# Performance work log

Measured on AMD Instinct MI355X. Metric: run time of the kernel, lower is better.

Reference implementation:

```python
import jax, jax.numpy as jnp
import numpy as np

LOSS_IDX = jnp.array([0, 1])    # loss_indices from __init__
BASIS_IDX = jnp.array([0, 1])   # dtw_mapping_basis (x, y)


def _dtw_path(cost):
    """Classic DTW DP + backtrack on cost [N, M].
    Returns padded alignment path (a, b) of length N+M-1 with validity mask.
    DP is run as an anti-diagonal wavefront scan (L = N+M-1 steps)."""
    N, M = cost.shape
    L = N + M - 1
    inf = jnp.float32(jnp.inf)
    i_idx = jnp.arange(N)

    def diag_step(carry, k):
        prev1, prev2 = carry  # diagonals k-1 and k-2, indexed by row i
        j = k - i_idx
        valid = (j >= 0) & (j < M)
        c = cost[i_idx, jnp.clip(j, 0, M - 1)]
        up = jnp.concatenate([jnp.full((1,), inf), prev1[:-1]])  # D[i-1, j]
        dg = jnp.concatenate([jnp.full((1,), inf), prev2[:-1]])  # D[i-1, j-1]
        lf = prev1                                               # D[i, j-1]
        best = jnp.minimum(jnp.minimum(up, dg), lf)
        best = jnp.where(jnp.isinf(best), jnp.float32(0.0), best)  # (0,0) seed
        cur = jnp.where(valid, c + best, inf)
        return (cur, prev1), cur

    init = (jnp.full((N,), inf), jnp.full((N,), inf))
    _, diags = jax.lax.scan(diag_step, init, jnp.arange(L))  # [L, N]: D[i,j] = diags[i+j, i]

    def getD(i, j):
        ok = (i >= 0) & (j >= 0)
        return jnp.where(ok, diags[jnp.clip(i + j, 0, L - 1), jnp.clip(i, 0, N - 1)], inf)

    def bt_step(carry, _):
        i, j, done = carry
        emit_valid = jnp.logical_not(done)
        cand = jnp.stack([getD(i - 1, j - 1), getD(i - 1, j), getD(i, j - 1)])
        m = jnp.argmin(cand)  # 0: diag, 1: up, 2: left
        ni = jnp.where(m == 2, i, i - 1)
        nj = jnp.where(m == 1, j, j - 1)
        done2 = done | ((i == 0) & (j == 0))
        ni = jnp.where(done2, 0, ni)
        nj = jnp.where(done2, 0, nj)
        return (ni, nj, done2), (i, j, emit_valid)

    init_bt = (jnp.int32(N - 1), jnp.int32(M - 1), jnp.bool_(False))
    _, (a, b, valid) = jax.lax.scan(bt_step, init_bt, None, length=L)
    return a, b, valid


def _dtw_loss_single(pred, targ, subcoef):
    # DTW alignment is computed on detached (numpy in torch) basis coords.
    p = jax.lax.stop_gradient(pred)[:, BASIS_IDX]
    t = jax.lax.stop_gradient(targ)[:, BASIS_IDX]
    # euclidean pairwise distance cost [N, M]
    cost = jnp.sqrt(jnp.sum((p[:, None, :] - t[None, :, :]) ** 2, axis=-1))
    a, b, valid = _dtw_path(cost)
    d = jnp.abs(pred[a][:, LOSS_IDX] - targ[b][:, LOSS_IDX]) * subcoef  # [L, 2]
    return jnp.sum(d * valid[:, None].astype(d.dtype))


def setup_inputs() -> dict:
    key = jax.random.key(0)
    k1, k2 = jax.random.split(key)
    B, N, M, F = 32, 1024, 1024, 4
    preds = jax.random.normal(k1, (B, N, F), dtype=jnp.float32)
    targs = jax.random.normal(k2, (B, M, F), dtype=jnp.float32)
    subcoef = jnp.ones((2,), dtype=jnp.float32)
    return {"preds": preds, "targs": targs, "subcoef": subcoef}


def reference(preds, targs, subcoef):
    per_sample = jax.vmap(_dtw_loss_single, in_axes=(0, 0, None))(preds, targs, subcoef)
    return jnp.sum(per_sample)
```

## Files before the change

### kernel.cpp

```cpp
#include <hip/hip_runtime.h>
#include <math.h>

#define BATCH 32
#define NN 1024
#define MM 1024
#define LPATH (NN + MM - 1)

#define PB 128
#define PQ 128
#define GB 8
#define GH 8
#define PAN_WORDS 1536
#define BAT_WORDS (GB * GH * PAN_WORDS)
#define DEC_WORDS ((size_t)BATCH * BAT_WORDS)
#define BR_OFFW DEC_WORDS
#define BRPL (9 * 1024)
#define FL_OFFW (BR_OFFW + (size_t)BATCH * BRPL)
#define WS_WORDS (FL_OFFW + (size_t)BATCH * 64)
#define REQ_WS_NEW (WS_WORDS * 4)

#define DEC_WORDS_PER_BATCH ((NN / 4) * (MM / 4))
#define REQ_WS ((size_t)BATCH * DEC_WORDS_PER_BATCH * 4)

__global__ void init_kernel(float* out) { out[0] = 0.0f; }

__global__ void init3(unsigned* __restrict__ wsu, float* __restrict__ out)
{
    const int t = threadIdx.x;
    if (t == 0) out[0] = 0.0f;
    for (int i = t; i < BATCH * 64; i += 256) wsu[FL_OFFW + i] = 0u;
}

__device__ __forceinline__ float wave_shr1(float v)
{
    return __int_as_float(__builtin_amdgcn_update_dpp(
        __float_as_int(v), __float_as_int(v), 0x138, 0xF, 0xF, false));
}

__global__ __launch_bounds__(64, 1) void dtw_dp(
    const float* __restrict__ preds, const float* __restrict__ targs,
    unsigned* __restrict__ wsu)
{
    const int blk = blockIdx.x;
    const int b = blk >> 3, r = blk & 7;
    const int l = threadIdx.x;
    const float INF = __builtin_inff();

    __shared__ __align__(16) float txA[1160], tyA[1160];
    __shared__ __align__(16) float TL[208];
    __shared__ __align__(16) float botL[128];

    for (int i = l; i < 64; i += 64) { txA[i] = 0.f; tyA[i] = 0.f; }
    for (int i = 1087 + l; i < 1160; i += 64) { txA[i] = 0.f; tyA[i] = 0.f; }
    if (l < 16) TL[192 + l] = INF;
    TL[128 + l] = INF;
    if (r == 0) { TL[l] = INF; TL[64 + l] = INF; }

    {
        const float4* tg4 = (const float4*)targs + (size_t)b * MM;
        #pragma unroll
        for (int k = 0; k < 4; ++k) {
            const float4 v = tg4[k * 64 + l];
            const int j = 63 + 4 * (k * 64 + l);
            txA[j] = v.x; tyA[j] = v.y;
            const float4 w = tg4[k * 64 + l];
            (void)w;
        }
    }
    {
        const float4* tg4 = (const float4*)targs + (size_t)b * MM;
        for (int j = l; j < MM; j += 64) {
            const float4 v = tg4[j];
            txA[63 + j] = v.x; tyA[63 + j] = v.y;
        }
    }

    const float4* pp4 = (const float4*)preds + (size_t)b * NN + r * PB;
    const float4 p0 = pp4[2 * l], p1 = pp4[2 * l + 1];
    const float px0 = p0.x, py0 = p0.y, px1 = p1.x, py1 = p1.y;

    unsigned* __restrict__ browI = wsu + BR_OFFW + (size_t)b * BRPL;
    unsigned* __restrict__ flagB = wsu + FL_OFFW + (size_t)b * 64;

    float D0 = INF, D1 = INF;
    __syncthreads();

    for (int c = 0; c < GH; ++c) {
        float tlm1;
        if (r > 0) {
            const int fi = (r - 1) * 8 + c;
            while (__hip_atomic_load(&flagB[fi], __ATOMIC_ACQUIRE,
                                     __HIP_MEMORY_SCOPE_AGENT) == 0u)
                __builtin_amdgcn_s_sleep(1);
            const unsigned* bp = browI + (size_t)r * 1024 + c * PQ;
            TL[2 * l] = __int_as_float(__hip_atomic_load(
                (unsigned*)&bp[2 * l], __ATOMIC_RELAXED, __HIP_MEMORY_SCOPE_AGENT));
            TL[2 * l + 1] = __int_as_float(__hip_atomic_load(
                (unsigned*)&bp[2 * l + 1], __ATOMIC_RELAXED, __HIP_MEMORY_SCOPE_AGENT));
            tlm1 = (c == 0) ? INF
                 : __int_as_float(__hip_atomic_load((unsigned*)&bp[-1],
                       __ATOMIC_RELAXED, __HIP_MEMORY_SCOPE_AGENT));
        } else {
            tlm1 = (c == 0) ? 0.0f : INF;
        }
        const float sh1 = wave_shr1(D1);
        const float dg0init = (l == 0) ? tlm1 : ((c == 0) ? INF : sh1);

        unsigned* __restrict__ decP = wsu + (size_t)b * BAT_WORDS
                                    + (size_t)(r * GH + c) * PAN_WORDS + l;
        const int cb = 63 + c * PQ;

        float txb[8], tyb[8];
        #pragma unroll
        for (int k = 0; k < 4; ++k) {
            txb[k] = txA[cb + k - l]; tyb[k] = tyA[cb + k - l];
        }
        float up0prev = INF;

        for (int it = 0; it < 24; ++it) {
            const int s0 = it * 8;
            const float4 T4a = *(const float4*)&TL[s0];
            const float4 T4b = *(const float4*)&TL[s0 + 4];
            const float Tv[8] = {T4a.x, T4a.y, T4a.z, T4a.w,
                                 T4b.x, T4b.y, T4b.z, T4b.w};
            unsigned word = 0;
            #pragma unroll
            for (int k = 0; k < 8; ++k) {
                const int s = s0 + k;
                const int jq = s - l;
                txb[(k + 4) & 7] = txA[cb + jq + 4];
                tyb[(k + 4) & 7] = tyA[cb + jq + 4];
                const float sh = wave_shr1(D1);
                const float up0 = (l == 0) ? Tv[k] : sh;
                const float dg0 = (jq == 0) ? dg0init : up0prev;
                const float tx = txb[k], ty = tyb[k];
                const float dx0 = px0 - tx, dy0 = py0 - ty;
                const float c0 = __builtin_amdgcn_sqrtf(dx0 * dx0 + dy0 * dy0);
                const float mn0 = fminf(dg0, fminf(up0, D0));
                const float D0n = c0 + mn0;
                const unsigned m0 = (mn0 == dg0) ? 0u : ((mn0 == up0) ? 1u : 2u);
                const float dg1 = D0;
                const float dx1 = px1 - tx, dy1 = py1 - ty;
                const float c1 = __builtin_amdgcn_sqrtf(dx1 * dx1 + dy1 * dy1);
                const float mn1 = fminf(dg1, fminf(D0n, D1));
                const float D1n = c1 + mn1;
                const unsigned m1 = (mn1 == dg1) ? 0u : ((mn1 == D0n) ? 1u : 2u);
                word |= (m0 | (m1 << 2)) << (4 * k);
                const bool act = (jq >= 0) && (jq < PQ);
                if (act) { D0 = D0n; D1 = D1n; }
                up0prev = up0;
                if (l == 63 && act) botL[jq] = D1n;
            }
            decP[it * 64] = word;
        }

        if (r < GB - 1) {
            unsigned* bw = browI + (size_t)(r + 1) * 1024 + c * PQ;
            __hip_atomic_store(&bw[2 * l], __float_as_int(botL[2 * l]),
                               __ATOMIC_RELAXED, __HIP_MEMORY_SCOPE_AGENT);
            __hip_atomic_store(&bw[2 * l + 1], __float_as_int(botL[2 * l + 1]),
                               __ATOMIC_RELAXED, __HIP_MEMORY_SCOPE_AGENT);
            __threadfence();
            if (l == 0)
                __hip_atomic_store(&flagB[r * 8 + c], 1u, __ATOMIC_RELEASE,
                                   __HIP_MEMORY_SCOPE_AGENT);
        }
    }
}

__global__ __launch_bounds__(256, 1) void dtw_bt(
    const float* __restrict__ preds, const float* __restrict__ targs,
    const float* __restrict__ subcoef, const float* __restrict__ ws,
    float* __restrict__ out)
{
    const int b = blockIdx.x, t = threadIdx.x;
    __shared__ float pxA[NN], pyA[NN], txA[MM], tyA[MM];
    __shared__ unsigned path[2048];
    __shared__ int sN;
    __shared__ float wsum[4];

    for (int it = 0; it < 4; ++it) {
        const int idx = it * 256 + t;
        const float4 p4 = ((const float4*)preds)[(size_t)b * NN + idx];
        pxA[idx] = p4.x; pyA[idx] = p4.y;
        const float4 t4 = ((const float4*)targs)[(size_t)b * MM + idx];
        txA[idx] = t4.x; tyA[idx] = t4.y;
    }
    __syncthreads();

    if (t == 0) {
        const unsigned* __restrict__ decB =
            (const unsigned*)ws + (size_t)b * BAT_WORDS;
        int i = NN - 1, j = MM - 1, n = 0;
        int cwidx = -1; unsigned cw = 0;
        while (true) {
            path[n++] = ((unsigned)i << 16) | (unsigned)j;
            if ((i | j) == 0) break;
            const int ll = (i & 127) >> 1;
            const int ss = ll + (j & 127);
            const int widx = (((i >> 7) << 3) + (j >> 7)) * PAN_WORDS
                           + (ss >> 3) * 64 + ll;
            if (widx != cwidx) { cw = decB[widx]; cwidx = widx; }
            const unsigned m = (cw >> ((ss & 7) * 4 + (i & 1) * 2)) & 3u;
            i -= (m != 2u); j -= (m != 1u);
        }
        sN = n;
    }
    __syncthreads();

    const float sc0 = subcoef[0], sc1 = subcoef[1];
    const int n = sN;
    float acc = 0.0f;
    for (int p = t; p < n; p += 256) {
        const unsigned e = path[p];
        const int i = (int)(e >> 16), j = (int)(e & 0xffffu);
        acc += fabsf(pxA[i] - txA[j]) * sc0 + fabsf(pyA[i] - tyA[j]) * sc1;
    }
    #pragma unroll
    for (int o = 32; o > 0; o >>= 1) acc += __shfl_down(acc, o);
    if ((t & 63) == 0) wsum[t >> 6] = acc;
    __syncthreads();
    if (t == 0) atomicAdd(out, (wsum[0] + wsum[1]) + (wsum[2] + wsum[3]));
}

__device__ inline void bt_walk4(const unsigned* __restrict__ sdec, int roff,
                                int iLow, int& i, int& j, int& n,
                                unsigned* __restrict__ path)
{
    int ri = i >> 2, jc = j >> 2;
    unsigned w = sdec[(ri - roff) * 256 + jc];
    while (true) {
        const int base = (ri - roff) * 256 + jc;
        const unsigned wl = sdec[(jc > 0)    ? base - 1   : base];
        const unsigned wu = sdec[(ri > roff) ? base - 256 : base];
        const unsigned wd = sdec[(ri > roff && jc > 0) ? base - 257 : base];
        bool done = false, susp = false;
        while (true) {
            path[n++] = ((unsigned)i << 16) | (unsigned)j;
            if ((i | j) == 0) { done = true; break; }
            const unsigned m = (w >> (((i & 3) * 4 + (j & 3)) * 2)) & 3u;
            i -= (m != 2u); j -= (m != 1u);
            if (i < iLow) { susp = true; break; }
            if ((i >> 2) != ri || (j >> 2) != jc) break;
        }
        if (done || susp) break;
        const int nri = i >> 2, njc = j >> 2;
        w = (nri == ri) ? wl : ((njc == jc) ? wu : wd);
        ri = nri; jc = njc;
    }
}

#define RRL 4
#define CCL 4
#define LANES 64
#define NWAVE 4
#define TPBL (MM / 4)
#define NSUP (TPBL + LANES - 1)
#define LAG 72
#define TOTL (NSUP + (NWAVE - 1) * LAG)
#define DEPTH 32

__global__ __launch_bounds__(256, 1) void dtw_fused_legacy(
    const float* __restrict__ preds, const float* __restrict__ targs,
    const float* __restrict__ subcoef, unsigned* __restrict__ dec,
    float* __restrict__ out)
{
    const int b = blockIdx.x, t = threadIdx.x;
    const int l = t & 63, w = t >> 6;
    const float INF = __builtin_inff();

    __shared__ float pxA[NN], pyA[NN], txA[MM], tyA[MM];
    __shared__ float4 ring[NWAVE - 1][DEPTH];
    __shared__ unsigned sdec[128 * 256];
    __shared__ unsigned path[LPATH + 1];
    __shared__ int sI, sJ, sN;
    __shared__ float wsum[NWAVE];

    for (int it = 0; it < NN / 256; ++it) {
        const int idx = it * 256 + t;
        const float4 p4 = ((const float4*)preds)[(size_t)b * NN + idx];
        pxA[idx] = p4.x; pyA[idx] = p4.y;
        const float4 t4 = ((const float4*)targs)[(size_t)b * MM + idx];
        txA[idx] = t4.x; tyA[idx] = t4.y;
    }
    __syncthreads();

    const int i0 = (w << 8) + (l << 2);
    const float4 px4 = ((const float4*)pxA)[i0 >> 2];
    const float4 py4 = ((const float4*)pyA)[i0 >> 2];
    const float px[RRL] = {px4.x, px4.y, px4.z, px4.w};
    const float py[RRL] = {py4.x, py4.y, py4.z, py4.w};
    unsigned* __restrict__ decW =
        dec + (size_t)b * DEC_WORDS_PER_BATCH + ((size_t)w << 14) + (size_t)l;

    float Dp[RRL], Dbot[CCL], bv[CCL];
    #pragma unroll
    for (int r = 0; r < RRL; ++r) Dp[r] = INF;
    #pragma unroll
    for (int c = 0; c < CCL; ++c) { Dbot[c] = INF; bv[c] = INF; }
    float bndRet = (w == 0 && l == 0) ? 0.0f : INF;
    float4 gcur = make_float4(INF, INF, INF, INF);
    float4 tx4 = ((const float4*)txA)[0], ty4 = ((const float4*)tyA)[0];
    const float4* __restrict__ ringR = ring[(w > 0) ? (w - 1) : 0];

    for (int u = 0; u < TOTL; ++u) {
        const int ul = u - LAG * w;
        if (l == 0) {
            const bool gb = (w > 0) && (ul >= 0) && (ul < TPBL);
            bv[0] = gb ? gcur.x : INF; bv[1] = gb ? gcur.y : INF;
            bv[2] = gb ? gcur.z : INF; bv[3] = gb ? gcur.w : INF;
        }
        const bool act = (ul >= l) && (ul < l + TPBL);
        if (act) {
            const float cx[CCL] = {tx4.x, tx4.y, tx4.z, tx4.w};
            const float cy[CCL] = {ty4.x, ty4.y, ty4.z, ty4.w};
            float cost[RRL][CCL];
            #pragma unroll
            for (int c = 0; c < CCL; ++c)
                #pragma unroll
                for (int r = 0; r < RRL; ++r) {
                    const float dx = px[r] - cx[c], dy = py[r] - cy[c];
                    cost[r][c] = __builtin_amdgcn_sqrtf(dx * dx + dy * dy);
                }
            unsigned word = 0;
            #pragma unroll
            for (int c = 0; c < CCL; ++c) {
                float up = bv[c];
                float dg = (c == 0) ? bndRet : bv[c - 1];
                #pragma unroll
                for (int r = 0; r < RRL; ++r) {
                    const float lf = Dp[r];
                    const unsigned m = (dg <= up && dg <= lf) ? 0u
                                     : ((up <= lf) ? 1u : 2u);
                    const float D = cost[r][c] + fminf(dg, fminf(up, lf));
                    word |= m << ((r * 4 + c) * 2);
                    dg = lf; up = D; Dp[r] = D;
                }
                Dbot[c] = up;
            }
            decW[(ul & 255) << 6] = word;
            if (l == LANES - 1 && w < NWAVE - 1)
                ring[w][ul & (DEPTH - 1)] =
                    make_float4(Dbot[0], Dbot[1], Dbot[2], Dbot[3]);
        }
        bndRet = bv[CCL - 1];
        #pragma unroll
        for (int c = 0; c < CCL; ++c) bv[c] = __shfl_up(Dbot[c], 1);
        const int un = ul + 1;
        if (un >= l && un < l + TPBL) {
            const int jn = CCL * (un - l);
            tx4 = ((const float4*)txA)[jn >> 2];
            ty4 = ((const float4*)tyA)[jn >> 2];
        }
        if (w > 0 && un >= 0 && un < TPBL)
            gcur = ringR[(un + 63) & (DEPTH - 1)];
        if ((u & 7) == 7) __syncthreads();
    }

    __threadfence_block();
    __syncthreads();

    const unsigned* __restrict__ decB = dec + (size_t)b * DEC_WORDS_PER_BATCH;
    {
        const uint4* g4 = (const uint4*)(decB + 32768);
        for (int k = t; k < 8192; k += 256) {
            const uint4 v = g4[k];
            const int kb = k << 2;
            const int wv = kb >> 14;
            const int rem = kb & 16383;
            const int q = rem >> 6;
            const int lb = rem & 63;
            const unsigned wd[4] = {v.x, v.y, v.z, v.w};
            #pragma unroll
            for (int e = 0; e < 4; ++e) {
                const int ll = lb + e;
                const int row = (wv << 6) + ll;
                const int jc = (q - ll) & 255;
                sdec[(row << 8) + jc] = wd[e];
            }
        }
    }
    __syncthreads();
    if (t == 0) {
        int i = NN - 1, j = MM - 1, n = 0;
        bt_walk4(sdec, 128, 512, i, j, n, path);
        sI = i; sJ = j; sN = n;
    }
    __syncthreads();
    {
        const uint4* g4 = (const uint4*)decB;
        for (int k = t; k < 8192; k += 256) {
            const uint4 v = g4[k];
            const int kb = k << 2;
            const int wv = kb >> 14;
            const int rem = kb & 16383;
            const int q = rem >> 6;
            const int lb = rem & 63;
            const unsigned wd[4] = {v.x, v.y, v.z, v.w};
            #pragma unroll
            for (int e = 0; e < 4; ++e) {
                const int ll = lb + e;
                const int row = (wv << 6) + ll;
                const int jc = (q - ll) & 255;
                sdec[(row << 8) + jc] = wd[e];
            }
        }
    }
    __syncthreads();
    if (t == 0) {
        int i = sI, j = sJ, n = sN;
        bt_walk4(sdec, 0, 0, i, j, n, path);
        sN = n;
    }
    __syncthreads();

    const float sc0 = subcoef[0], sc1 = subcoef[1];
    const int n = sN;
    float acc = 0.0f;
    for (int p = t; p < n; p += 256) {
        const unsigned e = path[p];
        const int i = (int)(e >> 16), j = (int)(e & 0xffffu);
        acc += fabsf(pxA[i] - txA[j]) * sc0 + fabsf(pyA[i] - tyA[j]) * sc1;
    }
    #pragma unroll
    for (int o = 32; o > 0; o >>= 1) acc += __shfl_down(acc, o);
    if ((t & 63) == 0) wsum[t >> 6] = acc;
    __syncthreads();
    if (t == 0) atomicAdd(out, (wsum[0] + wsum[1]) + (wsum[2] + wsum[3]));
}

__global__ __launch_bounds__(256) void dtw_fallback(
    const float* __restrict__ preds, const float* __restrict__ targs,
    const float* __restrict__ subcoef, unsigned* __restrict__ dec,
    float* __restrict__ out)
{
    const int b = blockIdx.x;
    const int t = threadIdx.x;
    const float INF = __builtin_inff();
    __shared__ float px[NN], py[NN];
    __shared__ float txy[2 * MM];
    __shared__ float bbuf[2][256];

    for (int it = 0; it < NN / 256; ++it) {
        const int idx = it * 256 + t;
        const float4 p4 = ((const float4*)preds)[(size_t)b * NN + idx];
        px[idx] = p4.x; py[idx] = p4.y;
        const float4 t4 = ((const float4*)targs)[(size_t)b * MM + idx];
        txy[2 * idx] = t4.x; txy[2 * idx + 1] = t4.y;
    }
    bbuf[0][t] = INF; bbuf[1][t] = INF;
    __syncthreads();

    float pxr[4], pyr[4], Dp[4];
    #pragma unroll
    for (int r = 0; r < 4; ++r) {
        pxr[r] = px[4 * t + r]; pyr[r] = py[4 * t + r]; Dp[r] = INF;
    }
    float dgB = (t == 0) ? 0.0f : INF;
    unsigned packed = 0;
    unsigned* decB = dec + (size_t)b * 65536;
    for (int s = 0; s < MM + 255; ++s) {
        const int j = s - t;
        const float upB = (t == 0) ? INF : bbuf[(s + 1) & 1][t - 1];
        if (j >= 0 && j < MM) {
            const float txj = txy[2 * j], tyj = txy[2 * j + 1];
            float up = upB, dg = dgB;
            unsigned mbits = 0;
            #pragma unroll
            for (int r = 0; r < 4; ++r) {
                const float dx = pxr[r] - txj, dy = pyr[r] - tyj;
                const float c = sqrtf(dx * dx + dy * dy);
                const float lf = Dp[r];
                const unsigned m = (dg <= up && dg <= lf) ? 0u
                                 : ((up <= lf) ? 1u : 2u);
                mbits |= m << (r * 8 + (j & 3) * 2);
                const float Dc = c + fminf(up, fminf(dg, lf));
                dg = lf; up = Dc; Dp[r] = Dc;
            }
            packed |= mbits;
            if ((j & 3) == 3) { decB[(unsigned)t * 256 + (j >> 2)] = packed; packed = 0; }
            bbuf[s & 1][t] = Dp[3];
        }
        dgB = upB;
        __syncthreads();
    }
    __threadfence_block();
    __syncthreads();
    if (t == 0) {
        const float sc0 = subcoef[0], sc1 = subcoef[1];
        int i = NN - 1, jj = MM - 1;
        float loss = 0.0f;
        int ti = i >> 2, tj = jj >> 2;
        unsigned wv = decB[ti * 256 + tj];
        while (true) {
            const int tjl = (tj > 0) ? tj - 1 : 0;
            const int til = (ti > 0) ? ti - 1 : 0;
            const unsigned wl = decB[ti * 256 + tjl];
            const unsigned wu = decB[til * 256 + tj];
            const unsigned wd = decB[til * 256 + tjl];
            bool done = false;
            while (true) {
                loss += fabsf(px[i] - txy[2 * jj]) * sc0
                      + fabsf(py[i] - txy[2 * jj + 1]) * sc1;
                if ((i | jj) == 0) { done = true; break; }
                const unsigned m = (wv >> (((i & 3) * 4 + (jj & 3)) * 2)) & 3u;
                i -= (m != 2u); jj -= (m != 1u);
                if ((i >> 2) != ti || (jj >> 2) != tj) break;
            }
            if (done) break;
            const int nti = i >> 2, ntj = jj >> 2;
            wv = (nti == ti) ? wl : ((ntj == tj) ? wu : wd);
            ti = nti; tj = ntj;
        }
        atomicAdd(out, loss);
    }
}

extern "C" void kernel_launch(void* const* d_in, const int* in_sizes, int n_in,
                              void* d_out, int out_size, void* d_ws, size_t ws_size,
                              hipStream_t stream) {
    const float* preds   = (const float*)d_in[0];
    const float* targs   = (const float*)d_in[1];
    const float* subcoef = (const float*)d_in[2];
    float* out = (float*)d_out;

    if (ws_size >= REQ_WS_NEW) {
        unsigned* wsu = (unsigned*)d_ws;
        init3<<<1, 256, 0, stream>>>(wsu, out);
        dtw_dp<<<BATCH * GB, 64, 0, stream>>>(preds, targs, wsu);
        dtw_bt<<<BATCH, 256, 0, stream>>>(preds, targs, subcoef,
                                          (const float*)d_ws, out);
    } else if (ws_size >= REQ_WS) {
        unsigned* dec = (unsigned*)d_ws;
        init_kernel<<<1, 1, 0, stream>>>(out);
        dtw_fused_legacy<<<BATCH, 256, 0, stream>>>(preds, targs, subcoef, dec, out);
    } else {
        unsigned* dec = (unsigned*)d_ws;
        init_kernel<<<1, 1, 0, stream>>>(out);
        dtw_fallback<<<BATCH, 256, 0, stream>>>(preds, targs, subcoef, dec, out);
    }
}
```

Before: 625.6 us.

## Interleave two batches per DP wavefront and prefetch backtrack decision words

```diff
diff --git a/kernel.cpp b/kernel.cpp
--- a/kernel.cpp
+++ b/kernel.cpp
@@ -37,132 +37,178 @@
         __float_as_int(v), __float_as_int(v), 0x138, 0xF, 0xF, false));
 }
 
-__global__ __launch_bounds__(64, 1) void dtw_dp(
+__global__ __launch_bounds__(64, 1) void dtw_dp2(
     const float* __restrict__ preds, const float* __restrict__ targs,
     unsigned* __restrict__ wsu)
 {
     const int blk = blockIdx.x;
-    const int b = blk >> 3, r = blk & 7;
+    const int p = blk >> 3, r = blk & 7;
+    const int b0 = 2 * p, b1 = 2 * p + 1;
     const int l = threadIdx.x;
     const float INF = __builtin_inff();
 
-    __shared__ __align__(16) float txA[1160], tyA[1160];
-    __shared__ __align__(16) float TL[208];
-    __shared__ __align__(16) float botL[128];
-
-    for (int i = l; i < 64; i += 64) { txA[i] = 0.f; tyA[i] = 0.f; }
-    for (int i = 1087 + l; i < 1160; i += 64) { txA[i] = 0.f; tyA[i] = 0.f; }
-    if (l < 16) TL[192 + l] = INF;
-    TL[128 + l] = INF;
-    if (r == 0) { TL[l] = INF; TL[64 + l] = INF; }
+    __shared__ __align__(16) float txA0[1160], tyA0[1160];
+    __shared__ __align__(16) float txA1[1160], tyA1[1160];
+    __shared__ __align__(16) float TL0[208], TL1[208];
+    __shared__ __align__(16) float botL0[128], botL1[128];
+
+    for (int i = l; i < 64; i += 64) {
+        txA0[i] = 0.f; tyA0[i] = 0.f; txA1[i] = 0.f; tyA1[i] = 0.f;
+    }
+    for (int i = 1087 + l; i < 1160; i += 64) {
+        txA0[i] = 0.f; tyA0[i] = 0.f; txA1[i] = 0.f; tyA1[i] = 0.f;
+    }
+    TL0[128 + l] = INF; TL1[128 + l] = INF;
+    if (l < 16) { TL0[192 + l] = INF; TL1[192 + l] = INF; }
+    if (r == 0) {
+        TL0[l] = INF; TL0[64 + l] = INF;
+        TL1[l] = INF; TL1[64 + l] = INF;
+    }
 
     {
-        const float4* tg4 = (const float4*)targs + (size_t)b * MM;
+        const float4* tg40 = (const float4*)targs + (size_t)b0 * MM;
+        const float4* tg41 = (const float4*)targs + (size_t)b1 * MM;
+        for (int j = l; j < MM; j += 64) {
+            const float4 v = tg40[j];
+            txA0[63 + j] = v.x; tyA0[63 + j] = v.y;
+            const float4 w = tg41[j];
+            txA1[63 + j] = w.x; tyA1[63 + j] = w.y;
+        }
+    }
+
+    const float4* pp40 = (const float4*)preds + (size_t)b0 * NN + r * PB;
+    const float4* pp41 = (const float4*)preds + (size_t)b1 * NN + r * PB;
+    const float4 a0 = pp40[2 * l], a1 = pp40[2 * l + 1];
+    const float4 c0v = pp41[2 * l], c1v = pp41[2 * l + 1];
+    const float pxA0 = a0.x, pyA0 = a0.y, pxA1 = a1.x, pyA1 = a1.y;
+    const float pxB0 = c0v.x, pyB0 = c0v.y, pxB1 = c1v.x, pyB1 = c1v.y;
+
+    unsigned* __restrict__ browI0 = wsu + BR_OFFW + (size_t)b0 * BRPL;
+    unsigned* __restrict__ browI1 = wsu + BR_OFFW + (size_t)b1 * BRPL;
+    unsigned* __restrict__ flagP = wsu + FL_OFFW + (size_t)p * 64;
+
+    float D0A = INF, D1A = INF, D0B = INF, D1B = INF;
+    __syncthreads();
+
+    for (int c = 0; c < GH; ++c) {
+        float tlm1A, tlm1B;
+        if (r > 0) {
+            const int fi = (r - 1) * 8 + c;
+            while (__hip_atomic_load(&flagP[fi], __ATOMIC_ACQUIRE,
+                                     __HIP_MEMORY_SCOPE_AGENT) == 0u)
+                __builtin_amdgcn_s_sleep(1);
+            const unsigned* bp0 = browI0 + (size_t)r * 1024 + c * PQ;
+            const unsigned* bp1 = browI1 + (size_t)r * 1024 + c * PQ;
+            TL0[2 * l] = __int_as_float(__hip_atomic_load((unsigned*)&bp0[2 * l],
+                             __ATOMIC_RELAXED, __HIP_MEMORY_SCOPE_AGENT));
+            TL0[2 * l + 1] = __int_as_float(__hip_atomic_load((unsigned*)&bp0[2 * l + 1],
+                             __ATOMIC_RELAXED, __HIP_MEMORY_SCOPE_AGENT));
+            TL1[2 * l] = __int_as_float(__hip_atomic_load((unsigned*)&bp1[2 * l],
+                             __ATOMIC_RELAXED, __HIP_MEMORY_SCOPE_AGENT));
+            TL1[2 * l + 1] = __int_as_float(__hip_atomic_load((unsigned*)&bp1[2 * l + 1],
+                             __ATOMIC_RELAXED, __HIP_MEMORY_SCOPE_AGENT));
+            tlm1A = (c == 0) ? INF
+                  : __int_as_float(__hip_atomic_load((unsigned*)&bp0[-1],
+                        __ATOMIC_RELAXED, __HIP_MEMORY_SCOPE_AGENT));
+            tlm1B = (c == 0) ? INF
+                  : __int_as_float(__hip_atomic_load((unsigned*)&bp1[-1],
+                        __ATOMIC_RELAXED, __HIP_MEMORY_SCOPE_AGENT));
+        } else {
+            tlm1A = (c == 0) ? 0.0f : INF;
+            tlm1B = (c == 0) ? 0.0f : INF;
+        }
+        const float shA1 = wave_shr1(D1A), shB1 = wave_shr1(D1B);
+        const float dg0initA = (l == 0) ? tlm1A : ((c == 0) ? INF : shA1);
+        const float dg0initB = (l == 0) ? tlm1B : ((c == 0) ? INF : shB1);
+
+        unsigned* __restrict__ decP0 = wsu + (size_t)b0 * BAT_WORDS
+                                     + (size_t)(r * GH + c) * PAN_WORDS + l;
+        unsigned* __restrict__ decP1 = wsu + (size_t)b1 * BAT_WORDS
+                                     + (size_t)(r * GH + c) * PAN_WORDS + l;
+        const int cb = 63 + c * PQ;
+
+        float txbA[8], tybA[8], txbB[8], tybB[8];
         #pragma unroll
         for (int k = 0; k < 4; ++k) {
-            const float4 v = tg4[k * 64 + l];
-            const int j = 63 + 4 * (k * 64 + l);
-            txA[j] = v.x; tyA[j] = v.y;
-            const float4 w = tg4[k * 64 + l];
-            (void)w;
-        }
-    }
-    {
-        const float4* tg4 = (const float4*)targs + (size_t)b * MM;
-        for (int j = l; j < MM; j += 64) {
-            const float4 v = tg4[j];
-            txA[63 + j] = v.x; tyA[63 + j] = v.y;
-        }
-    }
-
-    const float4* pp4 = (const float4*)preds + (size_t)b * NN + r * PB;
-    const float4 p0 = pp4[2 * l], p1 = pp4[2 * l + 1];
-    const float px0 = p0.x, py0 = p0.y, px1 = p1.x, py1 = p1.y;
-
-    unsigned* __restrict__ browI = wsu + BR_OFFW + (size_t)b * BRPL;
-    unsigned* __restrict__ flagB = wsu + FL_OFFW + (size_t)b * 64;
-
-    float D0 = INF, D1 = INF;
-    __syncthreads();
-
-    for (int c = 0; c < GH; ++c) {
-        float tlm1;
-        if (r > 0) {
-            const int fi = (r - 1) * 8 + c;
-            while (__hip_atomic_load(&flagB[fi], __ATOMIC_ACQUIRE,
-                                     __HIP_MEMORY_SCOPE_AGENT) == 0u)
-                __builtin_amdgcn_s_sleep(1);
-            const unsigned* bp = browI + (size_t)r * 1024 + c * PQ;
-            TL[2 * l] = __int_as_float(__hip_atomic_load(
-                (unsigned*)&bp[2 * l], __ATOMIC_RELAXED, __HIP_MEMORY_SCOPE_AGENT));
-            TL[2 * l + 1] = __int_as_float(__hip_atomic_load(
-                (unsigned*)&bp[2 * l + 1], __ATOMIC_RELAXED, __HIP_MEMORY_SCOPE_AGENT));
-            tlm1 = (c == 0) ? INF
-                 : __int_as_float(__hip_atomic_load((unsigned*)&bp[-1],
-                       __ATOMIC_RELAXED, __HIP_MEMORY_SCOPE_AGENT));
-        } else {
-            tlm1 = (c == 0) ? 0.0f : INF;
-        }
-        const float sh1 = wave_shr1(D1);
-        const float dg0init = (l == 0) ? tlm1 : ((c == 0) ? INF : sh1);
-
-        unsigned* __restrict__ decP = wsu + (size_t)b * BAT_WORDS
-                                    + (size_t)(r * GH + c) * PAN_WORDS + l;
-        const int cb = 63 + c * PQ;
-
-        float txb[8], tyb[8];
-        #pragma unroll
-        for (int k = 0; k < 4; ++k) {
-            txb[k] = txA[cb + k - l]; tyb[k] = tyA[cb + k - l];
-        }
-        float up0prev = INF;
+            txbA[k] = txA0[cb + k - l]; tybA[k] = tyA0[cb + k - l];
+            txbB[k] = txA1[cb + k - l]; tybB[k] = tyA1[cb + k - l];
+        }
+        float up0prevA = INF, up0prevB = INF;
 
         for (int it = 0; it < 24; ++it) {
             const int s0 = it * 8;
-            const float4 T4a = *(const float4*)&TL[s0];
-            const float4 T4b = *(const float4*)&TL[s0 + 4];
-            const float Tv[8] = {T4a.x, T4a.y, T4a.z, T4a.w,
-                                 T4b.x, T4b.y, T4b.z, T4b.w};
-            unsigned word = 0;
+            const float4 TA4a = *(const float4*)&TL0[s0];
+            const float4 TA4b = *(const float4*)&TL0[s0 + 4];
+            const float TvA[8] = {TA4a.x, TA4a.y, TA4a.z, TA4a.w,
+                                  TA4b.x, TA4b.y, TA4b.z, TA4b.w};
+            const float4 TB4a = *(const float4*)&TL1[s0];
+            const float4 TB4b = *(const float4*)&TL1[s0 + 4];
+            const float TvB[8] = {TB4a.x, TB4a.y, TB4a.z, TB4a.w,
+                                  TB4b.x, TB4b.y, TB4b.z, TB4b.w};
+            unsigned wordA = 0, wordB = 0;
             #pragma unroll
             for (int k = 0; k < 8; ++k) {
                 const int s = s0 + k;
                 const int jq = s - l;
-                txb[(k + 4) & 7] = txA[cb + jq + 4];
-                tyb[(k + 4) & 7] = tyA[cb + jq + 4];
-                const float sh = wave_shr1(D1);
-                const float up0 = (l == 0) ? Tv[k] : sh;
-                const float dg0 = (jq == 0) ? dg0init : up0prev;
-                const float tx = txb[k], ty = tyb[k];
-                const float dx0 = px0 - tx, dy0 = py0 - ty;
-                const float c0 = __builtin_amdgcn_sqrtf(dx0 * dx0 + dy0 * dy0);
-                const float mn0 = fminf(dg0, fminf(up0, D0));
-                const float D0n = c0 + mn0;
-                const unsigned m0 = (mn0 == dg0) ? 0u : ((mn0 == up0) ? 1u : 2u);
-                const float dg1 = D0;
-                const float dx1 = px1 - tx, dy1 = py1 - ty;
-                const float c1 = __builtin_amdgcn_sqrtf(dx1 * dx1 + dy1 * dy1);
-                const float mn1 = fminf(dg1, fminf(D0n, D1));
-                const float D1n = c1 + mn1;
-                const unsigned m1 = (mn1 == dg1) ? 0u : ((mn1 == D0n) ? 1u : 2u);
-                word |= (m0 | (m1 << 2)) << (4 * k);
+                txbA[(k + 4) & 7] = txA0[cb + jq + 4];
+                tybA[(k + 4) & 7] = tyA0[cb + jq + 4];
+                txbB[(k + 4) & 7] = txA1[cb + jq + 4];
+                tybB[(k + 4) & 7] = tyA1[cb + jq + 4];
                 const bool act = (jq >= 0) && (jq < PQ);
-                if (act) { D0 = D0n; D1 = D1n; }
-                up0prev = up0;
-                if (l == 63 && act) botL[jq] = D1n;
+                const float shA = wave_shr1(D1A);
+                const float up0A = (l == 0) ? TvA[k] : shA;
+                const float dg0A = (jq == 0) ? dg0initA : up0prevA;
+                const float txa = txbA[k], tya = tybA[k];
+                const float dxA0 = pxA0 - txa, dyA0 = pyA0 - tya;
+                const float cA0 = __builtin_amdgcn_sqrtf(dxA0 * dxA0 + dyA0 * dyA0);
+                const float mnA0 = fminf(dg0A, fminf(up0A, D0A));
+                const float DA0n = cA0 + mnA0;
+                const unsigned mA0 = (mnA0 == dg0A) ? 0u : ((mnA0 == up0A) ? 1u : 2u);
+                const float dgA1 = D0A;
+                const float dxA1 = pxA1 - txa, dyA1 = pyA1 - tya;
+                const float cA1 = __builtin_amdgcn_sqrtf(dxA1 * dxA1 + dyA1 * dyA1);
+                const float mnA1 = fminf(dgA1, fminf(DA0n, D1A));
+                const float DA1n = cA1 + mnA1;
+                const unsigned mA1 = (mnA1 == dgA1) ? 0u : ((mnA1 == DA0n) ? 1u : 2u);
+                wordA |= (mA0 | (mA1 << 2)) << (4 * k);
+                const float shB = wave_shr1(D1B);
+                const float up0B = (l == 0) ? TvB[k] : shB;
+                const float dg0B = (jq == 0) ? dg0initB : up0prevB;
+                const float txbv = txbB[k], tybv = tybB[k];
+                const float dxB0 = pxB0 - txbv, dyB0 = pyB0 - tybv;
+                const float cB0 = __builtin_amdgcn_sqrtf(dxB0 * dxB0 + dyB0 * dyB0);
+                const float mnB0 = fminf(dg0B, fminf(up0B, D0B));
+                const float DB0n = cB0 + mnB0;
+                const unsigned mB0 = (mnB0 == dg0B) ? 0u : ((mnB0 == up0B) ? 1u : 2u);
+                const float dgB1 = D0B;
+                const float dxB1 = pxB1 - txbv, dyB1 = pyB1 - tybv;
+                const float cB1 = __builtin_amdgcn_sqrtf(dxB1 * dxB1 + dyB1 * dyB1);
+                const float mnB1 = fminf(dgB1, fminf(DB0n, D1B));
+                const float DB1n = cB1 + mnB1;
+                const unsigned mB1 = (mnB1 == dgB1) ? 0u : ((mnB1 == DB0n) ? 1u : 2u);
+                wordB |= (mB0 | (mB1 << 2)) << (4 * k);
+                if (act) { D0A = DA0n; D1A = DA1n; D0B = DB0n; D1B = DB1n; }
+                up0prevA = up0A; up0prevB = up0B;
+                if (l == 63 && act) { botL0[jq] = DA1n; botL1[jq] = DB1n; }
             }
-            decP[it * 64] = word;
+            decP0[it * 64] = wordA;
+            decP1[it * 64] = wordB;
         }
 
         if (r < GB - 1) {
-            unsigned* bw = browI + (size_t)(r + 1) * 1024 + c * PQ;
-            __hip_atomic_store(&bw[2 * l], __float_as_int(botL[2 * l]),
+            unsigned* bw0 = browI0 + (size_t)(r + 1) * 1024 + c * PQ;
+            unsigned* bw1 = browI1 + (size_t)(r + 1) * 1024 + c * PQ;
+            __hip_atomic_store(&bw0[2 * l], __float_as_int(botL0[2 * l]),
                                __ATOMIC_RELAXED, __HIP_MEMORY_SCOPE_AGENT);
-            __hip_atomic_store(&bw[2 * l + 1], __float_as_int(botL[2 * l + 1]),
+            __hip_atomic_store(&bw0[2 * l + 1], __float_as_int(botL0[2 * l + 1]),
+                               __ATOMIC_RELAXED, __HIP_MEMORY_SCOPE_AGENT);
+            __hip_atomic_store(&bw1[2 * l], __float_as_int(botL1[2 * l]),
+                               __ATOMIC_RELAXED, __HIP_MEMORY_SCOPE_AGENT);
+            __hip_atomic_store(&bw1[2 * l + 1], __float_as_int(botL1[2 * l + 1]),
                                __ATOMIC_RELAXED, __HIP_MEMORY_SCOPE_AGENT);
             __threadfence();
             if (l == 0)
-                __hip_atomic_store(&flagB[r * 8 + c], 1u, __ATOMIC_RELEASE,
+                __hip_atomic_store(&flagP[r * 8 + c], 1u, __ATOMIC_RELEASE,
                                    __HIP_MEMORY_SCOPE_AGENT);
         }
     }
@@ -192,17 +238,36 @@
         const unsigned* __restrict__ decB =
             (const unsigned*)ws + (size_t)b * BAT_WORDS;
         int i = NN - 1, j = MM - 1, n = 0;
-        int cwidx = -1; unsigned cw = 0;
+        int cwidx; unsigned cw, wA, wB, wC;
+        {
+            const int ll = (i & 127) >> 1;
+            const int ss = ll + (j & 127);
+            cwidx = (((i >> 7) << 3) + (j >> 7)) * PAN_WORDS + (ss >> 3) * 64 + ll;
+            cw = decB[cwidx];
+            wA = decB[(cwidx >= 1) ? cwidx - 1 : 0];
+            wB = decB[(cwidx >= 64) ? cwidx - 64 : 0];
+            wC = decB[(cwidx >= 65) ? cwidx - 65 : 0];
+        }
         while (true) {
             path[n++] = ((unsigned)i << 16) | (unsigned)j;
             if ((i | j) == 0) break;
-            const int ll = (i & 127) >> 1;
-            const int ss = ll + (j & 127);
-            const int widx = (((i >> 7) << 3) + (j >> 7)) * PAN_WORDS
-                           + (ss >> 3) * 64 + ll;
-            if (widx != cwidx) { cw = decB[widx]; cwidx = widx; }
+            const int ss = ((i & 127) >> 1) + (j & 127);
             const unsigned m = (cw >> ((ss & 7) * 4 + (i & 1) * 2)) & 3u;
             i -= (m != 2u); j -= (m != 1u);
+            const int ll2 = (i & 127) >> 1;
+            const int ss2 = ll2 + (j & 127);
+            const int widx = (((i >> 7) << 3) + (j >> 7)) * PAN_WORDS
+                           + (ss2 >> 3) * 64 + ll2;
+            if (widx != cwidx) {
+                cw = (widx == cwidx - 1) ? wA
+                   : (widx == cwidx - 64) ? wB
+                   : (widx == cwidx - 65) ? wC
+                   : decB[widx];
+                cwidx = widx;
+                wA = decB[(widx >= 1) ? widx - 1 : 0];
+                wB = decB[(widx >= 64) ? widx - 64 : 0];
+                wC = decB[(widx >= 65) ? widx - 65 : 0];
+            }
         }
         sN = n;
     }
@@ -527,7 +592,7 @@
     if (ws_size >= REQ_WS_NEW) {
         unsigned* wsu = (unsigned*)d_ws;
         init3<<<1, 256, 0, stream>>>(wsu, out);
-        dtw_dp<<<BATCH * GB, 64, 0, stream>>>(preds, targs, wsu);
+        dtw_dp2<<<(BATCH / 2) * GB, 64, 0, stream>>>(preds, targs, wsu);
         dtw_bt<<<BATCH, 256, 0, stream>>>(preds, targs, subcoef,
                                           (const float*)d_ws, out);
     } else if (ws_size >= REQ_WS) {
```

Result: slower. 809.0 us (+29.3%).

## Stream DTW row-band sweep continuously with fine-grained 32-column boundary handoff

Applied to the files above, without the earlier changes.

```diff
diff --git a/kernel.cpp b/kernel.cpp
--- a/kernel.cpp
+++ b/kernel.cpp
@@ -7,28 +7,27 @@
 #define LPATH (NN + MM - 1)
 
 #define PB 128
-#define PQ 128
 #define GB 8
-#define GH 8
-#define PAN_WORDS 1536
-#define BAT_WORDS (GB * GH * PAN_WORDS)
-#define DEC_WORDS ((size_t)BATCH * BAT_WORDS)
-#define BR_OFFW DEC_WORDS
-#define BRPL (9 * 1024)
-#define FL_OFFW (BR_OFFW + (size_t)BATCH * BRPL)
-#define WS_WORDS (FL_OFFW + (size_t)BATCH * 64)
-#define REQ_WS_NEW (WS_WORDS * 4)
+#define SB 34
+#define BAND_WORDS (136 * 64)
+#define BAT_WORDS3 (GB * BAND_WORDS)
+#define DEC3_WORDS ((size_t)BATCH * BAT_WORDS3)
+#define BR3_OFFW DEC3_WORDS
+#define BR3_SZ ((size_t)BATCH * GB * 1024)
+#define CNT_OFFW (BR3_OFFW + BR3_SZ)
+#define WS3_WORDS (CNT_OFFW + BATCH * GB)
+#define REQ_WS3 (WS3_WORDS * 4)
 
 #define DEC_WORDS_PER_BATCH ((NN / 4) * (MM / 4))
 #define REQ_WS ((size_t)BATCH * DEC_WORDS_PER_BATCH * 4)
 
 __global__ void init_kernel(float* out) { out[0] = 0.0f; }
 
-__global__ void init3(unsigned* __restrict__ wsu, float* __restrict__ out)
+__global__ void init4(unsigned* __restrict__ wsu, float* __restrict__ out)
 {
     const int t = threadIdx.x;
     if (t == 0) out[0] = 0.0f;
-    for (int i = t; i < BATCH * 64; i += 256) wsu[FL_OFFW + i] = 0u;
+    if (t < BATCH * GB) wsu[CNT_OFFW + t] = 0u;
 }
 
 __device__ __forceinline__ float wave_shr1(float v)
@@ -37,7 +36,7 @@
         __float_as_int(v), __float_as_int(v), 0x138, 0xF, 0xF, false));
 }
 
-__global__ __launch_bounds__(64, 1) void dtw_dp(
+__global__ __launch_bounds__(64, 1) void dtw_dp3(
     const float* __restrict__ preds, const float* __restrict__ targs,
     unsigned* __restrict__ wsu)
 {
@@ -47,26 +46,13 @@
     const float INF = __builtin_inff();
 
     __shared__ __align__(16) float txA[1160], tyA[1160];
-    __shared__ __align__(16) float TL[208];
-    __shared__ __align__(16) float botL[128];
-
-    for (int i = l; i < 64; i += 64) { txA[i] = 0.f; tyA[i] = 0.f; }
+    __shared__ __align__(16) float TLb[2][32];
+    __shared__ float botL[64];
+
+    txA[l] = 0.f; tyA[l] = 0.f;
     for (int i = 1087 + l; i < 1160; i += 64) { txA[i] = 0.f; tyA[i] = 0.f; }
-    if (l < 16) TL[192 + l] = INF;
-    TL[128 + l] = INF;
-    if (r == 0) { TL[l] = INF; TL[64 + l] = INF; }
-
-    {
-        const float4* tg4 = (const float4*)targs + (size_t)b * MM;
-        #pragma unroll
-        for (int k = 0; k < 4; ++k) {
-            const float4 v = tg4[k * 64 + l];
-            const int j = 63 + 4 * (k * 64 + l);
-            txA[j] = v.x; tyA[j] = v.y;
-            const float4 w = tg4[k * 64 + l];
-            (void)w;
-        }
-    }
+    if (l < 32) { TLb[0][l] = INF; TLb[1][l] = INF; }
+
     {
         const float4* tg4 = (const float4*)targs + (size_t)b * MM;
         for (int j = l; j < MM; j += 64) {
@@ -74,66 +60,63 @@
             txA[63 + j] = v.x; tyA[63 + j] = v.y;
         }
     }
-
     const float4* pp4 = (const float4*)preds + (size_t)b * NN + r * PB;
     const float4 p0 = pp4[2 * l], p1 = pp4[2 * l + 1];
     const float px0 = p0.x, py0 = p0.y, px1 = p1.x, py1 = p1.y;
 
-    unsigned* __restrict__ browI = wsu + BR_OFFW + (size_t)b * BRPL;
-    unsigned* __restrict__ flagB = wsu + FL_OFFW + (size_t)b * 64;
+    unsigned* __restrict__ decBand =
+        wsu + (size_t)b * BAT_WORDS3 + (size_t)r * BAND_WORDS;
+    float* browAll = (float*)(wsu + BR3_OFFW);
+    const float* browPrev = browAll + ((size_t)b * GB + ((r > 0) ? r - 1 : 0)) * 1024;
+    float* browMine = browAll + ((size_t)b * GB + r) * 1024;
+    unsigned* cntPrev = wsu + CNT_OFFW + b * GB + ((r > 0) ? r - 1 : 0);
+    unsigned* cntMine = wsu + CNT_OFFW + b * GB + r;
 
     float D0 = INF, D1 = INF;
-    __syncthreads();
-
-    for (int c = 0; c < GH; ++c) {
-        float tlm1;
-        if (r > 0) {
-            const int fi = (r - 1) * 8 + c;
-            while (__hip_atomic_load(&flagB[fi], __ATOMIC_ACQUIRE,
-                                     __HIP_MEMORY_SCOPE_AGENT) == 0u)
-                __builtin_amdgcn_s_sleep(1);
-            const unsigned* bp = browI + (size_t)r * 1024 + c * PQ;
-            TL[2 * l] = __int_as_float(__hip_atomic_load(
-                (unsigned*)&bp[2 * l], __ATOMIC_RELAXED, __HIP_MEMORY_SCOPE_AGENT));
-            TL[2 * l + 1] = __int_as_float(__hip_atomic_load(
-                (unsigned*)&bp[2 * l + 1], __ATOMIC_RELAXED, __HIP_MEMORY_SCOPE_AGENT));
-            tlm1 = (c == 0) ? INF
-                 : __int_as_float(__hip_atomic_load((unsigned*)&bp[-1],
-                       __ATOMIC_RELAXED, __HIP_MEMORY_SCOPE_AGENT));
-        } else {
-            tlm1 = (c == 0) ? 0.0f : INF;
-        }
-        const float sh1 = wave_shr1(D1);
-        const float dg0init = (l == 0) ? tlm1 : ((c == 0) ? INF : sh1);
-
-        unsigned* __restrict__ decP = wsu + (size_t)b * BAT_WORDS
-                                    + (size_t)(r * GH + c) * PAN_WORDS + l;
-        const int cb = 63 + c * PQ;
-
-        float txb[8], tyb[8];
+    float up0prev = INF;
+    const float dg0init = (l == 0) ? ((r == 0) ? 0.0f : INF) : INF;
+    __syncthreads();
+
+    if (r > 0) {
+        while (__hip_atomic_load(cntPrev, __ATOMIC_ACQUIRE,
+                                 __HIP_MEMORY_SCOPE_AGENT) < 1u)
+            __builtin_amdgcn_s_sleep(1);
+        if (l < 32)
+            TLb[0][l] = __int_as_float(__hip_atomic_load(
+                (const unsigned*)&browPrev[l],
+                __ATOMIC_RELAXED, __HIP_MEMORY_SCOPE_AGENT));
+        __syncthreads();
+    }
+
+    float curx[8], cury[8], nxtx[8], nxty[8];
+    #pragma unroll
+    for (int k = 0; k < 8; ++k) {
+        curx[k] = txA[63 + k - l]; cury[k] = tyA[63 + k - l];
+    }
+
+    for (int c = 0; c < SB; ++c) {
         #pragma unroll
-        for (int k = 0; k < 4; ++k) {
-            txb[k] = txA[cb + k - l]; tyb[k] = tyA[cb + k - l];
-        }
-        float up0prev = INF;
-
-        for (int it = 0; it < 24; ++it) {
-            const int s0 = it * 8;
-            const float4 T4a = *(const float4*)&TL[s0];
-            const float4 T4b = *(const float4*)&TL[s0 + 4];
+        for (int m = 0; m < 4; ++m) {
+            const int u0 = 32 * c + 8 * m;
+            #pragma unroll
+            for (int k = 0; k < 8; ++k) {
+                nxtx[k] = txA[63 + (u0 + 8 + k) - l];
+                nxty[k] = tyA[63 + (u0 + 8 + k) - l];
+            }
+            const float4 T4a = *(const float4*)&TLb[c & 1][8 * m];
+            const float4 T4b = *(const float4*)&TLb[c & 1][8 * m + 4];
             const float Tv[8] = {T4a.x, T4a.y, T4a.z, T4a.w,
                                  T4b.x, T4b.y, T4b.z, T4b.w};
             unsigned word = 0;
             #pragma unroll
             for (int k = 0; k < 8; ++k) {
-                const int s = s0 + k;
-                const int jq = s - l;
-                txb[(k + 4) & 7] = txA[cb + jq + 4];
-                tyb[(k + 4) & 7] = tyA[cb + jq + 4];
+                const int u = u0 + k;
+                const int jq = u - l;
+                const bool act = (jq >= 0) && (jq < MM);
                 const float sh = wave_shr1(D1);
                 const float up0 = (l == 0) ? Tv[k] : sh;
                 const float dg0 = (jq == 0) ? dg0init : up0prev;
-                const float tx = txb[k], ty = tyb[k];
+                const float tx = curx[k], ty = cury[k];
                 const float dx0 = px0 - tx, dy0 = py0 - ty;
                 const float c0 = __builtin_amdgcn_sqrtf(dx0 * dx0 + dy0 * dy0);
                 const float mn0 = fminf(dg0, fminf(up0, D0));
@@ -146,31 +129,41 @@
                 const float D1n = c1 + mn1;
                 const unsigned m1 = (mn1 == dg1) ? 0u : ((mn1 == D0n) ? 1u : 2u);
                 word |= (m0 | (m1 << 2)) << (4 * k);
-                const bool act = (jq >= 0) && (jq < PQ);
                 if (act) { D0 = D0n; D1 = D1n; }
                 up0prev = up0;
-                if (l == 63 && act) botL[jq] = D1n;
-            }
-            decP[it * 64] = word;
-        }
-
-        if (r < GB - 1) {
-            unsigned* bw = browI + (size_t)(r + 1) * 1024 + c * PQ;
-            __hip_atomic_store(&bw[2 * l], __float_as_int(botL[2 * l]),
-                               __ATOMIC_RELAXED, __HIP_MEMORY_SCOPE_AGENT);
-            __hip_atomic_store(&bw[2 * l + 1], __float_as_int(botL[2 * l + 1]),
-                               __ATOMIC_RELAXED, __HIP_MEMORY_SCOPE_AGENT);
+                if (l == 63 && act) botL[jq & 63] = D1n;
+            }
+            decBand[(u0 >> 3) * 64 + l] = word;
+            #pragma unroll
+            for (int k = 0; k < 8; ++k) { curx[k] = nxtx[k]; cury[k] = nxty[k]; }
+        }
+        if (r < GB - 1 && c >= 2) {
+            const int ch = c - 2;
+            if (l < 32)
+                __hip_atomic_store((unsigned*)&browMine[32 * ch + l],
+                    __float_as_uint(botL[(32 * ch + l) & 63]),
+                    __ATOMIC_RELAXED, __HIP_MEMORY_SCOPE_AGENT);
             __threadfence();
             if (l == 0)
-                __hip_atomic_store(&flagB[r * 8 + c], 1u, __ATOMIC_RELEASE,
-                                   __HIP_MEMORY_SCOPE_AGENT);
+                __hip_atomic_store(cntMine, (unsigned)(ch + 1),
+                                   __ATOMIC_RELEASE, __HIP_MEMORY_SCOPE_AGENT);
+        }
+        const int k1 = c + 1;
+        if (r > 0 && k1 <= 31) {
+            while (__hip_atomic_load(cntPrev, __ATOMIC_ACQUIRE,
+                                     __HIP_MEMORY_SCOPE_AGENT) < (unsigned)(k1 + 1))
+                __builtin_amdgcn_s_sleep(1);
+            if (l < 32)
+                TLb[k1 & 1][l] = __int_as_float(__hip_atomic_load(
+                    (const unsigned*)&browPrev[32 * k1 + l],
+                    __ATOMIC_RELAXED, __HIP_MEMORY_SCOPE_AGENT));
         }
     }
 }
 
 __global__ __launch_bounds__(256, 1) void dtw_bt(
     const float* __restrict__ preds, const float* __restrict__ targs,
-    const float* __restrict__ subcoef, const float* __restrict__ ws,
+    const float* __restrict__ subcoef, const unsigned* __restrict__ wsu,
     float* __restrict__ out)
 {
     const int b = blockIdx.x, t = threadIdx.x;
@@ -189,17 +182,15 @@
     __syncthreads();
 
     if (t == 0) {
-        const unsigned* __restrict__ decB =
-            (const unsigned*)ws + (size_t)b * BAT_WORDS;
+        const unsigned* __restrict__ decB = wsu + (size_t)b * BAT_WORDS3;
         int i = NN - 1, j = MM - 1, n = 0;
         int cwidx = -1; unsigned cw = 0;
         while (true) {
             path[n++] = ((unsigned)i << 16) | (unsigned)j;
             if ((i | j) == 0) break;
             const int ll = (i & 127) >> 1;
-            const int ss = ll + (j & 127);
-            const int widx = (((i >> 7) << 3) + (j >> 7)) * PAN_WORDS
-                           + (ss >> 3) * 64 + ll;
+            const int ss = ll + j;
+            const int widx = (i >> 7) * BAND_WORDS + (ss >> 3) * 64 + ll;
             if (widx != cwidx) { cw = decB[widx]; cwidx = widx; }
             const unsigned m = (cw >> ((ss & 7) * 4 + (i & 1) * 2)) & 3u;
             i -= (m != 2u); j -= (m != 1u);
@@ -524,12 +515,11 @@
     const float* subcoef = (const float*)d_in[2];
     float* out = (float*)d_out;
 
-    if (ws_size >= REQ_WS_NEW) {
+    if (ws_size >= REQ_WS3) {
         unsigned* wsu = (unsigned*)d_ws;
-        init3<<<1, 256, 0, stream>>>(wsu, out);
-        dtw_dp<<<BATCH * GB, 64, 0, stream>>>(preds, targs, wsu);
-        dtw_bt<<<BATCH, 256, 0, stream>>>(preds, targs, subcoef,
-                                          (const float*)d_ws, out);
+        init4<<<1, 256, 0, stream>>>(wsu, out);
+        dtw_dp3<<<BATCH * GB, 64, 0, stream>>>(preds, targs, wsu);
+        dtw_bt<<<BATCH, 256, 0, stream>>>(preds, targs, subcoef, wsu, out);
     } else if (ws_size >= REQ_WS) {
         unsigned* dec = (unsigned*)d_ws;
         init_kernel<<<1, 1, 0, stream>>>(out);
```

After: 674.1 us. +7.7%, slower.
